# Kernel tuning notes

Measured on AMD Instinct MI355X. Metric: run time of the kernel, lower is better.

Reference implementation:

```python
import jax, jax.numpy as jnp
import numpy as np

ALPHA = 0.2  # leaky_relu negative slope
NEG_INF = -9e15


def gat_layer(h_in, W, a, adj_mask):
    """One GATLayer (eval mode, dropout disabled).
    h_in: [N, F_in], W: [F_in, F_out], a: [2*F_out, 1], adj_mask: [N, N] bool.
    Equivalent to the torch repeat/cat construction: e_ij = leaky_relu(a1.h_i + a2.h_j).
    """
    h = h_in @ W                          # [N, F_out]
    F_out = W.shape[1]
    a1 = a[:F_out, 0]                     # [F_out]
    a2 = a[F_out:, 0]                     # [F_out]
    f1 = h @ a1                           # [N]
    f2 = h @ a2                           # [N]
    e = jax.nn.leaky_relu(f1[:, None] + f2[None, :], negative_slope=ALPHA)  # [N, N]
    e = jnp.where(adj_mask, e, NEG_INF)
    attn = jax.nn.softmax(e, axis=-1)     # rows sum to 1
    return jax.nn.elu(attn @ h)           # [N, F_out]


def setup_inputs() -> dict:
    key = jax.random.key(0)
    ks = jax.random.split(key, 6)
    N, F_in, F_hid, F_out, H = 8192, 29, 8, 2, 4
    x = jax.random.normal(ks[0], (N, F_in), dtype=jnp.float32)
    adj = jax.random.randint(ks[1], (N, N), 0, 2, dtype=jnp.int32)
    # xavier_uniform with gain=1.414
    def xavier(k, shape, gain=1.414):
        fan_in, fan_out = shape[0], shape[1]
        bound = gain * np.sqrt(6.0 / (fan_in + fan_out))
        return jax.random.uniform(k, shape, jnp.float32, -bound, bound)
    W_heads = jnp.stack([xavier(k, (F_in, F_hid)) for k in jax.random.split(ks[2], H)])   # [H, 29, 8]
    a_heads = jnp.stack([xavier(k, (2 * F_hid, 1)) for k in jax.random.split(ks[3], H)])  # [H, 16, 1]
    W_out = xavier(ks[4], (F_hid * H, F_out))   # [32, 2]
    a_out = xavier(ks[5], (2 * F_out, 1))       # [4, 1]
    return {"x": x, "adj": adj, "W_heads": W_heads, "a_heads": a_heads,
            "W_out": W_out, "a_out": a_out}


def reference(x, adj, W_heads, a_heads, W_out, a_out):
    adj_mask = adj > 0
    heads = jax.vmap(lambda W, a: gat_layer(x, W, a, adj_mask))(W_heads, a_heads)  # [H, N, 8]
    hcat = jnp.concatenate(list(heads), axis=1)   # [N, H*8] (same order as torch cat over heads)
    out = gat_layer(hcat, W_out, a_out, adj_mask)  # [N, 2]
    return jax.nn.log_softmax(out, axis=1)
```

## Files before the change

kernel.cpp:

```cpp
#include <hip/hip_runtime.h>
#include <math.h>

#define N 8192
#define NW 128
#define FIN 29
#define FH 8
#define NH 4
#define ALPHA 0.2f
#define LOG2E 1.4426950408889634f
#define JS 4
#define JRR (N / JS)
#define JS2 4

typedef unsigned long long ull;
typedef unsigned short u16;
typedef __attribute__((ext_vector_type(8))) short bf16x8;
typedef __attribute__((ext_vector_type(4))) float f32x4;

__device__ inline unsigned bf16rn(float f) {
    unsigned u = __float_as_uint(f);
    return (u + 0x7fffu + ((u >> 16) & 1u)) >> 16;
}
__device__ inline unsigned fenc(float x) {
    unsigned u = __float_as_uint(x);
    return (u & 0x80000000u) ? ~u : (u | 0x80000000u);
}
__device__ inline float fdec(unsigned e) {
    return __uint_as_float((e & 0x80000000u) ? (e & 0x7fffffffu) : ~e);
}

__global__ void k0_pack(const int* __restrict__ adj, ull* __restrict__ mask,
                        unsigned* __restrict__ amax) {
    int row = blockIdx.x;
    int tid = threadIdx.x;
    int lane = tid & 63;
    int wave = tid >> 6;
    if (row == 0 && tid < 8) amax[tid] = 0u;
    const int* rp = adj + (size_t)row * N;
#pragma unroll 8
    for (int i = 0; i < 32; i++) {
        int a = rp[i * 256 + tid];
        ull b = __ballot(a > 0);
        if (lane == 0) mask[(size_t)row * NW + i * 4 + wave] = b;
    }
}

__global__ __launch_bounds__(64) void k1_feat(
    const float* __restrict__ x, const float* __restrict__ Wh,
    const float* __restrict__ ah,
    float2* __restrict__ e2, u16* __restrict__ Ht,
    float* __restrict__ f1a, unsigned* __restrict__ amax) {
    __shared__ float sW[NH * FIN * FH];
    __shared__ float sa[NH * 2 * FH];
    int tid = threadIdx.x;
    for (int i = tid; i < NH * FIN * FH; i += 64) sW[i] = Wh[i];
    for (int i = tid; i < NH * 2 * FH; i += 64) sa[i] = ah[i];
    __syncthreads();
    int node = blockIdx.x * 64 + tid;
    float xr[FIN];
#pragma unroll
    for (int f = 0; f < FIN; f++) xr[f] = x[node * FIN + f];
    float f2v[NH];
#pragma unroll
    for (int h = 0; h < NH; h++) {
        float hv[FH];
#pragma unroll
        for (int k = 0; k < FH; k++) {
            float s = 0.f;
#pragma unroll
            for (int f = 0; f < FIN; f++) s += xr[f] * sW[(h * FIN + f) * FH + k];
            hv[k] = s;
        }
        float f1 = 0.f, f2 = 0.f;
#pragma unroll
        for (int k = 0; k < FH; k++) {
            f1 += hv[k] * sa[h * 16 + k];
            f2 += hv[k] * sa[h * 16 + 8 + k];
        }
        float f1L = f1 * LOG2E, f2L = f2 * LOG2E;
        f2v[h] = f2L;
        f1a[node * 4 + h] = f1L;
        e2[h * N + node] = make_float2(__builtin_amdgcn_exp2f(f2L),
                                       __builtin_amdgcn_exp2f(ALPHA * f2L));
#pragma unroll
        for (int k = 0; k < FH; k++)
            Ht[(size_t)(h * 9 + k) * N + node] = (u16)bf16rn(hv[k]);
        Ht[(size_t)(h * 9 + 8) * N + node] = 0x3F80u;
    }
#pragma unroll
    for (int h = 0; h < NH; h++) {
        float v = f2v[h];
        for (int off = 32; off > 0; off >>= 1) v = fmaxf(v, __shfl_xor(v, off, 64));
        if (tid == 0) atomicMax(&amax[h], fenc(v));
    }
}

__global__ __launch_bounds__(256) void k3_attn1(
    const ull* __restrict__ mask, const float2* __restrict__ e2,
    const u16* __restrict__ Ht, const float* __restrict__ f1a,
    const unsigned* __restrict__ amax, float* __restrict__ part1) {
    __shared__ __align__(16) float2 sE2[JRR];
    int tid = threadIdx.x;
    int lane = tid & 63;
    int wave = tid >> 6;
    int h = blockIdx.x & 3;
    int js = (blockIdx.x >> 2) & 3;
    int rowblk = blockIdx.x >> 4;
    int jbase = js * JRR;

    {
        const float4* src = (const float4*)(e2 + (size_t)h * N + jbase);
        float4* dst = (float4*)sE2;
#pragma unroll
        for (int i = 0; i < (JRR / 2) / 256; i++)
            dst[tid + i * 256] = src[tid + i * 256];
    }

    int c = lane & 15;
    int kb = lane >> 4;
    int sh = kb * 8;
    int r = rowblk * 64 + wave * 16 + c;

    float mfL = fdec(amax[h]);
    float f1 = f1a[r * 4 + h];
    float v = f1 + mfL, m = fmaxf(v, ALPHA * v);
    float e1p = __builtin_amdgcn_exp2f(f1 - m);
    float e1n = __builtin_amdgcn_exp2f(ALPHA * f1 - m);

    const ull* mrow = mask + (size_t)r * NW + (jbase >> 6);
    const char* bbase = (const char*)(Ht + ((size_t)(h * 9 + c) * N + jbase + kb * 8));

    f32x4 acc = {0.f, 0.f, 0.f, 0.f};
    __syncthreads();

    for (int t = 0; t < JRR / 64; t++) {
        ull mw = mrow[t];
        unsigned mlo = (unsigned)mw;
        unsigned mhi = (unsigned)(mw >> 32);
#pragma unroll
        for (int hf = 0; hf < 2; hf++) {
            unsigned sw = (hf ? mhi : mlo) >> sh;
            const float4* qp = (const float4*)(sE2 + t * 64 + hf * 32 + kb * 8);
            float4 q0 = qp[0], q1 = qp[1], q2 = qp[2], q3 = qp[3];
            float w0 = fmaxf(e1p * q0.x, e1n * q0.y);
            float w1 = fmaxf(e1p * q0.z, e1n * q0.w);
            float w2 = fmaxf(e1p * q1.x, e1n * q1.y);
            float w3 = fmaxf(e1p * q1.z, e1n * q1.w);
            float w4 = fmaxf(e1p * q2.x, e1n * q2.y);
            float w5 = fmaxf(e1p * q2.z, e1n * q2.w);
            float w6 = fmaxf(e1p * q3.x, e1n * q3.y);
            float w7 = fmaxf(e1p * q3.z, e1n * q3.w);
            w0 = (sw & 1u)   ? w0 : 0.f;
            w1 = (sw & 2u)   ? w1 : 0.f;
            w2 = (sw & 4u)   ? w2 : 0.f;
            w3 = (sw & 8u)   ? w3 : 0.f;
            w4 = (sw & 16u)  ? w4 : 0.f;
            w5 = (sw & 32u)  ? w5 : 0.f;
            w6 = (sw & 64u)  ? w6 : 0.f;
            w7 = (sw & 128u) ? w7 : 0.f;
            uint4 ap;
            asm("v_cvt_pk_bf16_f32 %0, %1, %2" : "=v"(ap.x) : "v"(w0), "v"(w1));
            asm("v_cvt_pk_bf16_f32 %0, %1, %2" : "=v"(ap.y) : "v"(w2), "v"(w3));
            asm("v_cvt_pk_bf16_f32 %0, %1, %2" : "=v"(ap.z) : "v"(w4), "v"(w5));
            asm("v_cvt_pk_bf16_f32 %0, %1, %2" : "=v"(ap.w) : "v"(w6), "v"(w7));
            uint4 bp = *(const uint4*)(bbase + t * 128 + hf * 64);
            acc = __builtin_amdgcn_mfma_f32_16x16x32_bf16(
                __builtin_bit_cast(bf16x8, ap), __builtin_bit_cast(bf16x8, bp),
                acc, 0, 0, 0);
        }
    }
    if (c <= 8) {
        int rowout = rowblk * 64 + wave * 16 + kb * 4;
        float* dst = part1 + (size_t)(js * 36 + h * 9 + c) * N + rowout;
        *(float4*)dst = make_float4(acc[0], acc[1], acc[2], acc[3]);
    }
}

__global__ void k3b_final(const float* __restrict__ part1, const float* __restrict__ Wo,
                          const float* __restrict__ ao,
                          float4* __restrict__ rec2, float* __restrict__ f1b,
                          unsigned* __restrict__ amax) {
    __shared__ float sW[64];
    __shared__ float sa[4];
    int tid = threadIdx.x;
    if (tid < 64) sW[tid] = Wo[tid];
    if (tid < 4) sa[tid] = ao[tid];
    __syncthreads();
    int row = blockIdx.x * 256 + tid;
    float hv[32];
#pragma unroll
    for (int h = 0; h < NH; h++) {
        float s[9];
#pragma unroll
        for (int cc = 0; cc < 9; cc++) {
            float acc = 0.f;
#pragma unroll
            for (int js = 0; js < JS; js++)
                acc += part1[(size_t)(js * 36 + h * 9 + cc) * N + row];
            s[cc] = acc;
        }
        float inv = 1.f / s[8];
#pragma unroll
        for (int k = 0; k < FH; k++) {
            float o = s[k] * inv;
            hv[h * 8 + k] = (o > 0.f) ? o : expm1f(o);
        }
    }
    float h0 = 0.f, h1 = 0.f;
#pragma unroll
    for (int i = 0; i < 32; i++) {
        h0 = fmaf(hv[i], sW[i * 2 + 0], h0);
        h1 = fmaf(hv[i], sW[i * 2 + 1], h1);
    }
    float f1 = (h0 * sa[0] + h1 * sa[1]) * LOG2E;
    float f2 = (h0 * sa[2] + h1 * sa[3]) * LOG2E;
    rec2[row] = make_float4(__builtin_amdgcn_exp2f(f2), h0, h1,
                            __builtin_amdgcn_exp2f(ALPHA * f2));
    f1b[row] = f1;
    float vmax = f2;
    for (int off = 32; off > 0; off >>= 1) vmax = fmaxf(vmax, __shfl_xor(vmax, off, 64));
    if ((tid & 63) == 0) atomicMax(&amax[4], fenc(vmax));
}

__global__ __launch_bounds__(256) void k6_attn2(
    const ull* __restrict__ mask, const float4* __restrict__ rec2,
    const float* __restrict__ f1b, const unsigned* __restrict__ amax,
    float* __restrict__ part2) {
    int tid = threadIdx.x;
    int lane = tid & 63;
    int wave = tid >> 6;
    int blk = blockIdx.x >> 2;
    int js = blockIdx.x & 3;
    int rbase = blk * 16 + wave * 4;
    const int JR = N / JS2;
    int jbase = js * JR;

    float mb = fdec(amax[4]);
    float e1p[4], e1n[4];
#pragma unroll
    for (int i = 0; i < 4; i++) {
        float f1 = f1b[rbase + i];
        float v = f1 + mb, m = fmaxf(v, ALPHA * v);
        e1p[i] = __builtin_amdgcn_exp2f(f1 - m);
        e1n[i] = __builtin_amdgcn_exp2f(ALPHA * f1 - m);
    }
    float a0[4] = {0.f, 0.f, 0.f, 0.f};
    float a1[4] = {0.f, 0.f, 0.f, 0.f};
    float dd[4] = {0.f, 0.f, 0.f, 0.f};
    const ull* mr[4];
#pragma unroll
    for (int i = 0; i < 4; i++) mr[i] = mask + (size_t)(rbase + i) * NW;

    int wb = jbase >> 6;
#pragma unroll 4
    for (int s = 0; s < JR / 64; s++) {
        float4 q = rec2[jbase + s * 64 + lane];
#pragma unroll
        for (int i = 0; i < 4; i++) {
            ull mw = mr[i][wb + s];
            float w = fmaxf(e1p[i] * q.x, e1n[i] * q.w);
            w = ((mw >> lane) & 1ull) ? w : 0.f;
            a0[i] = fmaf(w, q.y, a0[i]);
            a1[i] = fmaf(w, q.z, a1[i]);
            dd[i] += w;
        }
    }
#pragma unroll
    for (int i = 0; i < 4; i++) {
        for (int off = 32; off > 0; off >>= 1) {
            a0[i] += __shfl_xor(a0[i], off, 64);
            a1[i] += __shfl_xor(a1[i], off, 64);
            dd[i] += __shfl_xor(dd[i], off, 64);
        }
    }
    if (lane == 0) {
#pragma unroll
        for (int i = 0; i < 4; i++) {
            int row = rbase + i;
            part2[(js * 3 + 0) * N + row] = a0[i];
            part2[(js * 3 + 1) * N + row] = a1[i];
            part2[(js * 3 + 2) * N + row] = dd[i];
        }
    }
}

__global__ void k6b_final(const float* __restrict__ part2, float* __restrict__ out) {
    int row = blockIdx.x * 256 + threadIdx.x;
    float s0 = 0.f, s1 = 0.f, d = 0.f;
#pragma unroll
    for (int js = 0; js < JS2; js++) {
        s0 += part2[(js * 3 + 0) * N + row];
        s1 += part2[(js * 3 + 1) * N + row];
        d  += part2[(js * 3 + 2) * N + row];
    }
    float inv = 1.f / d;
    float e0 = s0 * inv, e1 = s1 * inv;
    e0 = (e0 > 0.f) ? e0 : expm1f(e0);
    e1 = (e1 > 0.f) ? e1 : expm1f(e1);
    float mx = fmaxf(e0, e1);
    float lse = mx + logf(expf(e0 - mx) + expf(e1 - mx));
    ((float2*)out)[row] = make_float2(e0 - lse, e1 - lse);
}

extern "C" void kernel_launch(void* const* d_in, const int* in_sizes, int n_in,
                              void* d_out, int out_size, void* d_ws, size_t ws_size,
                              hipStream_t stream) {
    const float* x   = (const float*)d_in[0];
    const int*   adj = (const int*)d_in[1];
    const float* Wh  = (const float*)d_in[2];
    const float* ah  = (const float*)d_in[3];
    const float* Wo  = (const float*)d_in[4];
    const float* ao  = (const float*)d_in[5];
    float* out = (float*)d_out;
    float* ws = (float*)d_ws;

    ull*      mask  = (ull*)ws;
    float2*   e2    = (float2*)(ws + 2097152);
    u16*      Ht    = (u16*)(ws + 2162688);
    float*    f1a   = ws + 2310144;
    float*    part1 = ws + 2342912;
    float4*   rec2  = (float4*)(ws + 3522560);
    float*    f1b   = ws + 3555328;
    float*    part2 = ws + 3563520;
    unsigned* amax  = (unsigned*)(ws + 3661824);

    k0_pack<<<N, 256, 0, stream>>>(adj, mask, amax);
    k1_feat<<<N / 64, 64, 0, stream>>>(x, Wh, ah, e2, Ht, f1a, amax);
    k3_attn1<<<(N / 64) * JS * NH, 256, 0, stream>>>(mask, e2, Ht, f1a, amax, part1);
    k3b_final<<<N / 256, 256, 0, stream>>>(part1, Wo, ao, rec2, f1b, amax);
    k6_attn2<<<(N / 16) * JS2, 256, 0, stream>>>(mask, rec2, f1b, amax, part2);
    k6b_final<<<N / 256, 256, 0, stream>>>(part2, out);
}
```

Baseline: 531.6 us.

## Pack B operand in MFMA fragment layout, two row tiles per wave, drop LDS staging

k1_feat now runs one thread per (node, head), stages x through LDS, and writes H into a pre-swizzled MFMA B-fragment layout padded to 16 columns. Each lane of k3_attn1 can then load its B fragment with one coalesced uint4. k3_attn1 now handles two 16-row tiles per wave, so every B fragment and e2 load serves two MFMAs, and the grid is halved. It also drops the LDS copy of e2 and reads it straight from global/L1, relying on cache hits instead of shared memory. The costs are higher register pressure, under a launch bound of 4 blocks, and a larger packed B buffer.

```diff
diff --git a/kernel.cpp b/kernel.cpp
--- a/kernel.cpp
+++ b/kernel.cpp
@@ -45,61 +45,61 @@
     }
 }
 
-__global__ __launch_bounds__(64) void k1_feat(
+__global__ __launch_bounds__(256) void k1_feat(
     const float* __restrict__ x, const float* __restrict__ Wh,
     const float* __restrict__ ah,
-    float2* __restrict__ e2, u16* __restrict__ Ht,
+    float2* __restrict__ e2, u16* __restrict__ Bpk,
     float* __restrict__ f1a, unsigned* __restrict__ amax) {
+    __shared__ float sx[64 * FIN];
     __shared__ float sW[NH * FIN * FH];
     __shared__ float sa[NH * 2 * FH];
     int tid = threadIdx.x;
-    for (int i = tid; i < NH * FIN * FH; i += 64) sW[i] = Wh[i];
-    for (int i = tid; i < NH * 2 * FH; i += 64) sa[i] = ah[i];
+    for (int i = tid; i < NH * FIN * FH; i += 256) sW[i] = Wh[i];
+    for (int i = tid; i < NH * 2 * FH; i += 256) sa[i] = ah[i];
+    for (int i = tid; i < 64 * FIN; i += 256) sx[i] = x[(size_t)blockIdx.x * 64 * FIN + i];
     __syncthreads();
-    int node = blockIdx.x * 64 + tid;
-    float xr[FIN];
-#pragma unroll
-    for (int f = 0; f < FIN; f++) xr[f] = x[node * FIN + f];
-    float f2v[NH];
-#pragma unroll
-    for (int h = 0; h < NH; h++) {
-        float hv[FH];
-#pragma unroll
-        for (int k = 0; k < FH; k++) {
-            float s = 0.f;
-#pragma unroll
-            for (int f = 0; f < FIN; f++) s += xr[f] * sW[(h * FIN + f) * FH + k];
-            hv[k] = s;
-        }
-        float f1 = 0.f, f2 = 0.f;
-#pragma unroll
-        for (int k = 0; k < FH; k++) {
-            f1 += hv[k] * sa[h * 16 + k];
-            f2 += hv[k] * sa[h * 16 + 8 + k];
-        }
-        float f1L = f1 * LOG2E, f2L = f2 * LOG2E;
-        f2v[h] = f2L;
-        f1a[node * 4 + h] = f1L;
-        e2[h * N + node] = make_float2(__builtin_amdgcn_exp2f(f2L),
-                                       __builtin_amdgcn_exp2f(ALPHA * f2L));
-#pragma unroll
-        for (int k = 0; k < FH; k++)
-            Ht[(size_t)(h * 9 + k) * N + node] = (u16)bf16rn(hv[k]);
-        Ht[(size_t)(h * 9 + 8) * N + node] = 0x3F80u;
-    }
-#pragma unroll
-    for (int h = 0; h < NH; h++) {
-        float v = f2v[h];
-        for (int off = 32; off > 0; off >>= 1) v = fmaxf(v, __shfl_xor(v, off, 64));
-        if (tid == 0) atomicMax(&amax[h], fenc(v));
-    }
-}
-
-__global__ __launch_bounds__(256) void k3_attn1(
+    int h = tid & 3;
+    int nl = tid >> 2;
+    int node = blockIdx.x * 64 + nl;
+    float hv[FH];
+#pragma unroll
+    for (int k = 0; k < FH; k++) {
+        float s = 0.f;
+#pragma unroll
+        for (int f = 0; f < FIN; f++) s += sx[nl * FIN + f] * sW[(h * FIN + f) * FH + k];
+        hv[k] = s;
+    }
+    float f1 = 0.f, f2 = 0.f;
+#pragma unroll
+    for (int k = 0; k < FH; k++) {
+        f1 += hv[k] * sa[h * 16 + k];
+        f2 += hv[k] * sa[h * 16 + 8 + k];
+    }
+    float f1L = f1 * LOG2E, f2L = f2 * LOG2E;
+    f1a[node * 4 + h] = f1L;
+    e2[(size_t)h * N + node] = make_float2(__builtin_amdgcn_exp2f(f2L),
+                                           __builtin_amdgcn_exp2f(ALPHA * f2L));
+    int js = node >> 11;
+    int t  = (node >> 6) & 31;
+    int hfl = (node >> 5) & 1;
+    int kb = (node >> 3) & 3;
+    int e  = node & 7;
+    u16* dst = Bpk + ((size_t)(((h * 4 + js) * 32 + t) * 2 + hfl)) * 512 + e;
+#pragma unroll
+    for (int cc = 0; cc < 16; cc++) {
+        u16 v = (cc < FH) ? (u16)bf16rn(hv[cc])
+                          : ((cc == 8) ? (u16)0x3F80u : (u16)0);
+        dst[(kb * 16 + cc) * 8] = v;
+    }
+    float v = f2L;
+    for (int off = 4; off < 64; off <<= 1) v = fmaxf(v, __shfl_xor(v, off, 64));
+    if ((tid & 63) < 4) atomicMax(&amax[tid & 3], fenc(v));
+}
+
+__global__ __launch_bounds__(256, 4) void k3_attn1(
     const ull* __restrict__ mask, const float2* __restrict__ e2,
-    const u16* __restrict__ Ht, const float* __restrict__ f1a,
+    const uint4* __restrict__ Bpk, const float* __restrict__ f1a,
     const unsigned* __restrict__ amax, float* __restrict__ part1) {
-    __shared__ __align__(16) float2 sE2[JRR];
     int tid = threadIdx.x;
     int lane = tid & 63;
     int wave = tid >> 6;
@@ -108,71 +108,99 @@
     int rowblk = blockIdx.x >> 4;
     int jbase = js * JRR;
 
-    {
-        const float4* src = (const float4*)(e2 + (size_t)h * N + jbase);
-        float4* dst = (float4*)sE2;
-#pragma unroll
-        for (int i = 0; i < (JRR / 2) / 256; i++)
-            dst[tid + i * 256] = src[tid + i * 256];
-    }
-
     int c = lane & 15;
     int kb = lane >> 4;
     int sh = kb * 8;
-    int r = rowblk * 64 + wave * 16 + c;
+    int r0 = rowblk * 128 + wave * 16 + c;
+    int r1 = r0 + 64;
 
     float mfL = fdec(amax[h]);
-    float f1 = f1a[r * 4 + h];
-    float v = f1 + mfL, m = fmaxf(v, ALPHA * v);
-    float e1p = __builtin_amdgcn_exp2f(f1 - m);
-    float e1n = __builtin_amdgcn_exp2f(ALPHA * f1 - m);
-
-    const ull* mrow = mask + (size_t)r * NW + (jbase >> 6);
-    const char* bbase = (const char*)(Ht + ((size_t)(h * 9 + c) * N + jbase + kb * 8));
-
-    f32x4 acc = {0.f, 0.f, 0.f, 0.f};
-    __syncthreads();
+    float f1 = f1a[r0 * 4 + h];
+    float vv = f1 + mfL, mm = fmaxf(vv, ALPHA * vv);
+    float e1p0 = __builtin_amdgcn_exp2f(f1 - mm);
+    float e1n0 = __builtin_amdgcn_exp2f(ALPHA * f1 - mm);
+    f1 = f1a[r1 * 4 + h];
+    vv = f1 + mfL; mm = fmaxf(vv, ALPHA * vv);
+    float e1p1 = __builtin_amdgcn_exp2f(f1 - mm);
+    float e1n1 = __builtin_amdgcn_exp2f(ALPHA * f1 - mm);
+
+    const ull* mr0 = mask + (size_t)r0 * NW + (jbase >> 6);
+    const ull* mr1 = mask + (size_t)r1 * NW + (jbase >> 6);
+    const float2* e2h = e2 + (size_t)h * N + jbase + kb * 8;
+    const uint4* bp0 = Bpk + (size_t)(h * 4 + js) * 4096 + lane;
+
+    f32x4 acc0 = {0.f, 0.f, 0.f, 0.f};
+    f32x4 acc1 = {0.f, 0.f, 0.f, 0.f};
 
     for (int t = 0; t < JRR / 64; t++) {
-        ull mw = mrow[t];
-        unsigned mlo = (unsigned)mw;
-        unsigned mhi = (unsigned)(mw >> 32);
+        ull mw0 = mr0[t];
+        ull mw1 = mr1[t];
 #pragma unroll
         for (int hf = 0; hf < 2; hf++) {
-            unsigned sw = (hf ? mhi : mlo) >> sh;
-            const float4* qp = (const float4*)(sE2 + t * 64 + hf * 32 + kb * 8);
+            const float4* qp = (const float4*)(e2h + t * 64 + hf * 32);
             float4 q0 = qp[0], q1 = qp[1], q2 = qp[2], q3 = qp[3];
-            float w0 = fmaxf(e1p * q0.x, e1n * q0.y);
-            float w1 = fmaxf(e1p * q0.z, e1n * q0.w);
-            float w2 = fmaxf(e1p * q1.x, e1n * q1.y);
-            float w3 = fmaxf(e1p * q1.z, e1n * q1.w);
-            float w4 = fmaxf(e1p * q2.x, e1n * q2.y);
-            float w5 = fmaxf(e1p * q2.z, e1n * q2.w);
-            float w6 = fmaxf(e1p * q3.x, e1n * q3.y);
-            float w7 = fmaxf(e1p * q3.z, e1n * q3.w);
-            w0 = (sw & 1u)   ? w0 : 0.f;
-            w1 = (sw & 2u)   ? w1 : 0.f;
-            w2 = (sw & 4u)   ? w2 : 0.f;
-            w3 = (sw & 8u)   ? w3 : 0.f;
-            w4 = (sw & 16u)  ? w4 : 0.f;
-            w5 = (sw & 32u)  ? w5 : 0.f;
-            w6 = (sw & 64u)  ? w6 : 0.f;
-            w7 = (sw & 128u) ? w7 : 0.f;
-            uint4 ap;
-            asm("v_cvt_pk_bf16_f32 %0, %1, %2" : "=v"(ap.x) : "v"(w0), "v"(w1));
-            asm("v_cvt_pk_bf16_f32 %0, %1, %2" : "=v"(ap.y) : "v"(w2), "v"(w3));
-            asm("v_cvt_pk_bf16_f32 %0, %1, %2" : "=v"(ap.z) : "v"(w4), "v"(w5));
-            asm("v_cvt_pk_bf16_f32 %0, %1, %2" : "=v"(ap.w) : "v"(w6), "v"(w7));
-            uint4 bp = *(const uint4*)(bbase + t * 128 + hf * 64);
-            acc = __builtin_amdgcn_mfma_f32_16x16x32_bf16(
-                __builtin_bit_cast(bf16x8, ap), __builtin_bit_cast(bf16x8, bp),
-                acc, 0, 0, 0);
+            uint4 bp = bp0[(t * 2 + hf) * 64];
+            unsigned sw0 = ((unsigned)(mw0 >> (hf * 32))) >> sh;
+            unsigned sw1 = ((unsigned)(mw1 >> (hf * 32))) >> sh;
+            {
+                float w0 = fmaxf(e1p0 * q0.x, e1n0 * q0.y);
+                float w1 = fmaxf(e1p0 * q0.z, e1n0 * q0.w);
+                float w2 = fmaxf(e1p0 * q1.x, e1n0 * q1.y);
+                float w3 = fmaxf(e1p0 * q1.z, e1n0 * q1.w);
+                float w4 = fmaxf(e1p0 * q2.x, e1n0 * q2.y);
+                float w5 = fmaxf(e1p0 * q2.z, e1n0 * q2.w);
+                float w6 = fmaxf(e1p0 * q3.x, e1n0 * q3.y);
+                float w7 = fmaxf(e1p0 * q3.z, e1n0 * q3.w);
+                w0 = (sw0 & 1u)   ? w0 : 0.f;
+                w1 = (sw0 & 2u)   ? w1 : 0.f;
+                w2 = (sw0 & 4u)   ? w2 : 0.f;
+                w3 = (sw0 & 8u)   ? w3 : 0.f;
+                w4 = (sw0 & 16u)  ? w4 : 0.f;
+                w5 = (sw0 & 32u)  ? w5 : 0.f;
+                w6 = (sw0 & 64u)  ? w6 : 0.f;
+                w7 = (sw0 & 128u) ? w7 : 0.f;
+                uint4 ap;
+                asm("v_cvt_pk_bf16_f32 %0, %1, %2" : "=v"(ap.x) : "v"(w0), "v"(w1));
+                asm("v_cvt_pk_bf16_f32 %0, %1, %2" : "=v"(ap.y) : "v"(w2), "v"(w3));
+                asm("v_cvt_pk_bf16_f32 %0, %1, %2" : "=v"(ap.z) : "v"(w4), "v"(w5));
+                asm("v_cvt_pk_bf16_f32 %0, %1, %2" : "=v"(ap.w) : "v"(w6), "v"(w7));
+                acc0 = __builtin_amdgcn_mfma_f32_16x16x32_bf16(
+                    __builtin_bit_cast(bf16x8, ap), __builtin_bit_cast(bf16x8, bp),
+                    acc0, 0, 0, 0);
+            }
+            {
+                float w0 = fmaxf(e1p1 * q0.x, e1n1 * q0.y);
+                float w1 = fmaxf(e1p1 * q0.z, e1n1 * q0.w);
+                float w2 = fmaxf(e1p1 * q1.x, e1n1 * q1.y);
+                float w3 = fmaxf(e1p1 * q1.z, e1n1 * q1.w);
+                float w4 = fmaxf(e1p1 * q2.x, e1n1 * q2.y);
+                float w5 = fmaxf(e1p1 * q2.z, e1n1 * q2.w);
+                float w6 = fmaxf(e1p1 * q3.x, e1n1 * q3.y);
+                float w7 = fmaxf(e1p1 * q3.z, e1n1 * q3.w);
+                w0 = (sw1 & 1u)   ? w0 : 0.f;
+                w1 = (sw1 & 2u)   ? w1 : 0.f;
+                w2 = (sw1 & 4u)   ? w2 : 0.f;
+                w3 = (sw1 & 8u)   ? w3 : 0.f;
+                w4 = (sw1 & 16u)  ? w4 : 0.f;
+                w5 = (sw1 & 32u)  ? w5 : 0.f;
+                w6 = (sw1 & 64u)  ? w6 : 0.f;
+                w7 = (sw1 & 128u) ? w7 : 0.f;
+                uint4 ap;
+                asm("v_cvt_pk_bf16_f32 %0, %1, %2" : "=v"(ap.x) : "v"(w0), "v"(w1));
+                asm("v_cvt_pk_bf16_f32 %0, %1, %2" : "=v"(ap.y) : "v"(w2), "v"(w3));
+                asm("v_cvt_pk_bf16_f32 %0, %1, %2" : "=v"(ap.z) : "v"(w4), "v"(w5));
+                asm("v_cvt_pk_bf16_f32 %0, %1, %2" : "=v"(ap.w) : "v"(w6), "v"(w7));
+                acc1 = __builtin_amdgcn_mfma_f32_16x16x32_bf16(
+                    __builtin_bit_cast(bf16x8, ap), __builtin_bit_cast(bf16x8, bp),
+                    acc1, 0, 0, 0);
+            }
         }
     }
     if (c <= 8) {
-        int rowout = rowblk * 64 + wave * 16 + kb * 4;
-        float* dst = part1 + (size_t)(js * 36 + h * 9 + c) * N + rowout;
-        *(float4*)dst = make_float4(acc[0], acc[1], acc[2], acc[3]);
+        int ro = rowblk * 128 + wave * 16 + kb * 4;
+        float* dst = part1 + (size_t)(js * 36 + h * 9 + c) * N + ro;
+        *(float4*)dst = make_float4(acc0[0], acc0[1], acc0[2], acc0[3]);
+        *(float4*)(dst + 64) = make_float4(acc1[0], acc1[1], acc1[2], acc1[3]);
     }
 }
 
@@ -316,17 +344,17 @@
 
     ull*      mask  = (ull*)ws;
     float2*   e2    = (float2*)(ws + 2097152);
-    u16*      Ht    = (u16*)(ws + 2162688);
-    float*    f1a   = ws + 2310144;
-    float*    part1 = ws + 2342912;
-    float4*   rec2  = (float4*)(ws + 3522560);
-    float*    f1b   = ws + 3555328;
-    float*    part2 = ws + 3563520;
-    unsigned* amax  = (unsigned*)(ws + 3661824);
+    u16*      Bpk   = (u16*)(ws + 2162688);
+    float*    f1a   = ws + 2424832;
+    float*    part1 = ws + 2457600;
+    float4*   rec2  = (float4*)(ws + 3637248);
+    float*    f1b   = ws + 3670016;
+    float*    part2 = ws + 3678208;
+    unsigned* amax  = (unsigned*)(ws + 3776512);
 
     k0_pack<<<N, 256, 0, stream>>>(adj, mask, amax);
-    k1_feat<<<N / 64, 64, 0, stream>>>(x, Wh, ah, e2, Ht, f1a, amax);
-    k3_attn1<<<(N / 64) * JS * NH, 256, 0, stream>>>(mask, e2, Ht, f1a, amax, part1);
+    k1_feat<<<N / 64, 256, 0, stream>>>(x, Wh, ah, e2, Bpk, f1a, amax);
+    k3_attn1<<<(N / 128) * JS * NH, 256, 0, stream>>>(mask, e2, (const uint4*)Bpk, f1a, amax, part1);
     k3b_final<<<N / 256, 256, 0, stream>>>(part1, Wo, ao, rec2, f1b, amax);
     k6_attn2<<<(N / 16) * JS2, 256, 0, stream>>>(mask, rec2, f1b, amax, part2);
     k6b_final<<<N / 256, 256, 0, stream>>>(part2, out);
```

Result: faster. 503.9 us (-5.2%).
